# Kernel optimization log

Measured on AMD Instinct MI355X. Metric: run time of the kernel, lower is better.

The kernel has to match this reference:

```python
import jax, jax.numpy as jnp
import numpy as np

EPS = 1e-8
TARGET_MARGIN = 2.0  # init kwarg
NEG_THRESH = 0.1

B, V, L_KO, L_EN, N_NEG = 256, 128000, 32, 32, 1024


def setup_inputs() -> dict:
    key = jax.random.key(0)
    k0, k1, k2, k3, k4, k5 = jax.random.split(key, 6)
    return {
        "sparse_rep": jax.random.uniform(k0, (B, V), dtype=jnp.float32),
        "ko_ids": jax.random.randint(k1, (B, L_KO), 0, V, dtype=jnp.int64),
        "ko_len": jax.random.randint(k2, (B,), 0, L_KO + 1, dtype=jnp.int32),
        "en_ids": jax.random.randint(k3, (B, L_EN), 0, V, dtype=jnp.int64),
        "en_len": jax.random.randint(k4, (B,), 0, L_EN + 1, dtype=jnp.int32),
        "non_target_ids": jax.random.randint(k5, (N_NEG,), 0, V, dtype=jnp.int64),
    }


def _masked_mean(vals, length):
    # vals: [B, L]; length: [B]. Per-sample mean over the first `length`
    # entries; 0 contribution when length == 0 (matches the torch skip).
    L = vals.shape[1]
    mask = jnp.arange(L)[None, :] < length[:, None]
    s = jnp.sum(jnp.where(mask, vals, 0.0), axis=1)
    cnt = jnp.maximum(length, 1).astype(vals.dtype)
    return jnp.where(length > 0, s / cnt, 0.0)  # [B]


def reference(sparse_rep, ko_ids, ko_len, en_ids, en_len, non_target_ids):
    # ragged gathers expressed as padded take_along_axis + mask
    ko_act = jnp.take_along_axis(sparse_rep, ko_ids, axis=1)  # [B, L_KO]
    en_act = jnp.take_along_axis(sparse_rep, en_ids, axis=1)  # [B, L_EN]

    self_loss = jnp.mean(_masked_mean(-jnp.log(ko_act + EPS), ko_len))
    target_loss = jnp.mean(_masked_mean(-jnp.log(en_act + EPS), en_len))
    margin_loss = jnp.mean(_masked_mean(jax.nn.relu(TARGET_MARGIN - en_act), en_len))

    neg_act = sparse_rep[:, non_target_ids]  # [B, N_NEG]
    negative_loss = jnp.mean(jax.nn.relu(neg_act - NEG_THRESH))

    # dict {'self','target','margin','negative'} stacked into a [4] array
    return jnp.stack([self_loss, target_loss, margin_loss, negative_loss])
```

## Files before the change

kernel.cpp:

```cpp
#include <hip/hip_runtime.h>
#include <hip/hip_bf16.h>

#define B_SZ   256
#define V_SZ   128000
#define L_KO   32
#define L_EN   32
#define N_NEG  1024
#define EPS_F  1e-8f
#define MARGIN 2.0f
#define NEG_TH 0.1f

__global__ __launch_bounds__(256) void term_loss_partial(
    const float* __restrict__ rep,
    const int*   __restrict__ ko_ids,
    const int*   __restrict__ ko_len,
    const int*   __restrict__ en_ids,
    const int*   __restrict__ en_len,
    const int*   __restrict__ neg_ids,
    float4*      __restrict__ partials)
{
    const int b   = blockIdx.x;
    const int tid = threadIdx.x;
    const float* __restrict__ row = rep + (size_t)b * V_SZ;

    float s_self = 0.0f, s_tgt = 0.0f, s_mar = 0.0f, s_neg = 0.0f;

    if (tid < 32) {
        if (tid < ko_len[b]) {
            const float v = row[ko_ids[b * L_KO + tid]];
            s_self = -logf(v + EPS_F);
        }
    } else if (tid < 64) {
        const int l = tid - 32;
        if (l < en_len[b]) {
            const float v = row[en_ids[b * L_EN + l]];
            s_tgt = -logf(v + EPS_F);
            s_mar = fmaxf(MARGIN - v, 0.0f);
        }
    }

    #pragma unroll
    for (int j = tid; j < N_NEG; j += 256) {
        const float v = row[neg_ids[j]];
        s_neg += fmaxf(v - NEG_TH, 0.0f);
    }

    #pragma unroll
    for (int off = 32; off > 0; off >>= 1) {
        s_self += __shfl_down(s_self, off, 64);
        s_tgt  += __shfl_down(s_tgt,  off, 64);
        s_mar  += __shfl_down(s_mar,  off, 64);
        s_neg  += __shfl_down(s_neg,  off, 64);
    }

    __shared__ float red[4][4];
    const int wave = tid >> 6;
    if ((tid & 63) == 0) {
        red[wave][0] = s_self;
        red[wave][1] = s_tgt;
        red[wave][2] = s_mar;
        red[wave][3] = s_neg;
    }
    __syncthreads();

    if (tid == 0) {
        float a0 = 0.0f, a1 = 0.0f, a2 = 0.0f, a3 = 0.0f;
        #pragma unroll
        for (int w = 0; w < 4; ++w) {
            a0 += red[w][0];
            a1 += red[w][1];
            a2 += red[w][2];
            a3 += red[w][3];
        }
        const int kl = ko_len[b];
        const int el = en_len[b];
        float4 p;
        p.x = (kl > 0) ? (a0 / (float)kl) : 0.0f;
        p.y = (el > 0) ? (a1 / (float)el) : 0.0f;
        p.z = (el > 0) ? (a2 / (float)el) : 0.0f;
        p.w = a3;
        partials[b] = p;
    }
}

__global__ __launch_bounds__(256) void term_loss_reduce(
    const float4* __restrict__ partials,
    float*        __restrict__ out)
{
    const int tid = threadIdx.x;
    float4 p = partials[tid];

    #pragma unroll
    for (int off = 32; off > 0; off >>= 1) {
        p.x += __shfl_down(p.x, off, 64);
        p.y += __shfl_down(p.y, off, 64);
        p.z += __shfl_down(p.z, off, 64);
        p.w += __shfl_down(p.w, off, 64);
    }

    __shared__ float4 red[4];
    const int wave = tid >> 6;
    if ((tid & 63) == 0) red[wave] = p;
    __syncthreads();

    if (tid == 0) {
        float4 a = red[0];
        #pragma unroll
        for (int w = 1; w < 4; ++w) {
            a.x += red[w].x;
            a.y += red[w].y;
            a.z += red[w].z;
            a.w += red[w].w;
        }
        out[0] = a.x * (1.0f / (float)B_SZ);
        out[1] = a.y * (1.0f / (float)B_SZ);
        out[2] = a.z * (1.0f / (float)B_SZ);
        out[3] = a.w * (1.0f / ((float)B_SZ * (float)N_NEG));
    }
}

extern "C" void kernel_launch(void* const* d_in, const int* in_sizes, int n_in,
                              void* d_out, int out_size, void* d_ws, size_t ws_size,
                              hipStream_t stream)
{
    const float* rep     = (const float*)d_in[0];
    const int*   ko_ids  = (const int*)  d_in[1];
    const int*   ko_len  = (const int*)  d_in[2];
    const int*   en_ids  = (const int*)  d_in[3];
    const int*   en_len  = (const int*)  d_in[4];
    const int*   neg_ids = (const int*)  d_in[5];
    float*       out     = (float*)d_out;
    float4*      part    = (float4*)d_ws;

    term_loss_partial<<<B_SZ, 256, 0, stream>>>(
        rep, ko_ids, ko_len, en_ids, en_len, neg_ids, part);
    term_loss_reduce<<<1, 256, 0, stream>>>(part, out);
}
```

Measured before the change: 178.1 us.

## Fuse partial and final reduction into one cooperative kernel with grid sync

Merges the per-row partial kernel and the single-block reduce kernel into one cooperative launch that uses a grid-wide sync before block 0 sums the partials. It also loads the negative ids as int4 so each thread issues its four gathers at once instead of looping. This is meant to remove the second kernel launch and the gap between the two kernels. In exchange it adds the cost of a cooperative launch and a grid barrier, which can be expensive on AMD hardware.

```diff
diff --git a/kernel.cpp b/kernel.cpp
--- a/kernel.cpp
+++ b/kernel.cpp
@@ -1,5 +1,7 @@
 #include <hip/hip_runtime.h>
-#include <hip/hip_bf16.h>
+#include <hip/hip_cooperative_groups.h>
+
+namespace cg = cooperative_groups;
 
 #define B_SZ   256
 #define V_SZ   128000
@@ -10,20 +12,27 @@
 #define MARGIN 2.0f
 #define NEG_TH 0.1f
 
-__global__ __launch_bounds__(256) void term_loss_partial(
+__global__ __launch_bounds__(256) void term_loss_fused(
     const float* __restrict__ rep,
     const int*   __restrict__ ko_ids,
     const int*   __restrict__ ko_len,
     const int*   __restrict__ en_ids,
     const int*   __restrict__ en_len,
     const int*   __restrict__ neg_ids,
-    float4*      __restrict__ partials)
+    float*       __restrict__ ws,
+    float*       __restrict__ out)
 {
     const int b   = blockIdx.x;
     const int tid = threadIdx.x;
     const float* __restrict__ row = rep + (size_t)b * V_SZ;
 
-    float s_self = 0.0f, s_tgt = 0.0f, s_mar = 0.0f, s_neg = 0.0f;
+    const int4 nid = ((const int4*)neg_ids)[tid];
+    float s_self = 0.0f, s_tgt = 0.0f, s_mar = 0.0f;
+    const float n0 = fmaxf(row[nid.x] - NEG_TH, 0.0f);
+    const float n1 = fmaxf(row[nid.y] - NEG_TH, 0.0f);
+    const float n2 = fmaxf(row[nid.z] - NEG_TH, 0.0f);
+    const float n3 = fmaxf(row[nid.w] - NEG_TH, 0.0f);
+    float s_neg = (n0 + n1) + (n2 + n3);
 
     if (tid < 32) {
         if (tid < ko_len[b]) {
@@ -40,12 +49,6 @@
     }
 
     #pragma unroll
-    for (int j = tid; j < N_NEG; j += 256) {
-        const float v = row[neg_ids[j]];
-        s_neg += fmaxf(v - NEG_TH, 0.0f);
-    }
-
-    #pragma unroll
     for (int off = 32; off > 0; off >>= 1) {
         s_self += __shfl_down(s_self, off, 64);
         s_tgt  += __shfl_down(s_tgt,  off, 64);
@@ -54,8 +57,10 @@
     }
 
     __shared__ float red[4][4];
+    __shared__ float fin[4][4];
     const int wave = tid >> 6;
-    if ((tid & 63) == 0) {
+    const int lane = tid & 63;
+    if (lane == 0) {
         red[wave][0] = s_self;
         red[wave][1] = s_tgt;
         red[wave][2] = s_mar;
@@ -74,48 +79,38 @@
         }
         const int kl = ko_len[b];
         const int el = en_len[b];
-        float4 p;
-        p.x = (kl > 0) ? (a0 / (float)kl) : 0.0f;
-        p.y = (el > 0) ? (a1 / (float)el) : 0.0f;
-        p.z = (el > 0) ? (a2 / (float)el) : 0.0f;
-        p.w = a3;
-        partials[b] = p;
-    }
-}
-
-__global__ __launch_bounds__(256) void term_loss_reduce(
-    const float4* __restrict__ partials,
-    float*        __restrict__ out)
-{
-    const int tid = threadIdx.x;
-    float4 p = partials[tid];
-
-    #pragma unroll
-    for (int off = 32; off > 0; off >>= 1) {
-        p.x += __shfl_down(p.x, off, 64);
-        p.y += __shfl_down(p.y, off, 64);
-        p.z += __shfl_down(p.z, off, 64);
-        p.w += __shfl_down(p.w, off, 64);
+        const float p0 = (kl > 0) ? (a0 / (float)kl) : 0.0f;
+        const float p1 = (el > 0) ? (a1 / (float)el) : 0.0f;
+        const float p2 = (el > 0) ? (a2 / (float)el) : 0.0f;
+        __hip_atomic_store(&ws[b * 4 + 0], p0, __ATOMIC_RELAXED, __HIP_MEMORY_SCOPE_AGENT);
+        __hip_atomic_store(&ws[b * 4 + 1], p1, __ATOMIC_RELAXED, __HIP_MEMORY_SCOPE_AGENT);
+        __hip_atomic_store(&ws[b * 4 + 2], p2, __ATOMIC_RELAXED, __HIP_MEMORY_SCOPE_AGENT);
+        __hip_atomic_store(&ws[b * 4 + 3], a3, __ATOMIC_RELAXED, __HIP_MEMORY_SCOPE_AGENT);
     }
 
-    __shared__ float4 red[4];
-    const int wave = tid >> 6;
-    if ((tid & 63) == 0) red[wave] = p;
-    __syncthreads();
+    cg::this_grid().sync();
 
-    if (tid == 0) {
-        float4 a = red[0];
+    if (b == 0) {
+        const int c  = tid & 3;
+        const int r0 = tid >> 2;
+        float v = 0.0f;
         #pragma unroll
-        for (int w = 1; w < 4; ++w) {
-            a.x += red[w].x;
-            a.y += red[w].y;
-            a.z += red[w].z;
-            a.w += red[w].w;
+        for (int k = 0; k < 4; ++k) {
+            v += __hip_atomic_load(&ws[(size_t)(r0 + 64 * k) * 4 + c],
+                                   __ATOMIC_RELAXED, __HIP_MEMORY_SCOPE_AGENT);
         }
-        out[0] = a.x * (1.0f / (float)B_SZ);
-        out[1] = a.y * (1.0f / (float)B_SZ);
-        out[2] = a.z * (1.0f / (float)B_SZ);
-        out[3] = a.w * (1.0f / ((float)B_SZ * (float)N_NEG));
+        #pragma unroll
+        for (int off = 32; off >= 4; off >>= 1)
+            v += __shfl_down(v, off, 64);
+        if (lane < 4) fin[wave][lane] = v;
+        __syncthreads();
+        if (tid < 4) {
+            const float a = fin[0][tid] + fin[1][tid] + fin[2][tid] + fin[3][tid];
+            const float scale = (tid == 3)
+                ? (1.0f / ((float)B_SZ * (float)N_NEG))
+                : (1.0f / (float)B_SZ);
+            out[tid] = a * scale;
+        }
     }
 }
 
@@ -130,9 +125,13 @@
     const int*   en_len  = (const int*)  d_in[4];
     const int*   neg_ids = (const int*)  d_in[5];
     float*       out     = (float*)d_out;
-    float4*      part    = (float4*)d_ws;
+    float*       ws      = (float*)d_ws;
 
-    term_loss_partial<<<B_SZ, 256, 0, stream>>>(
-        rep, ko_ids, ko_len, en_ids, en_len, neg_ids, part);
-    term_loss_reduce<<<1, 256, 0, stream>>>(part, out);
+    void* args[] = {
+        (void*)&rep, (void*)&ko_ids, (void*)&ko_len,
+        (void*)&en_ids, (void*)&en_len, (void*)&neg_ids,
+        (void*)&ws, (void*)&out
+    };
+    hipLaunchCooperativeKernel((const void*)term_loss_fused,
+                               dim3(B_SZ), dim3(256), args, 0, stream);
 }
```

Result: slower. 225.6 us (+26.7%).
